# Optimization experiments

Measured on AMD Instinct MI355X. Metric: run time of the kernel, lower is better.

The kernel has to match this reference:

```python
import jax, jax.numpy as jnp
import numpy as np

N = 100000      # nodes
E = 3200000     # edges (avg degree 32)
NFEAT, NHID, NCLASS = 512, 256, 64


def setup_inputs() -> dict:
    key = jax.random.key(0)
    ks = jax.random.split(key, 10)
    x = jax.random.normal(ks[0], (N, NFEAT), dtype=jnp.float32)
    src = jax.random.randint(ks[1], (E,), 0, N, dtype=jnp.int32)
    dst = jax.random.randint(ks[2], (E,), 0, N, dtype=jnp.int32)
    # normalized-adjacency-style positive edge weights
    edge_weight = jax.random.uniform(ks[3], (E,), dtype=jnp.float32) / 32.0
    stdv1 = 1.0 / np.sqrt(NHID)
    stdv2 = 1.0 / np.sqrt(NCLASS)
    W1 = jax.random.uniform(ks[4], (NFEAT, NHID), minval=-stdv1, maxval=stdv1, dtype=jnp.float32)
    b1 = jnp.zeros((NHID,), jnp.float32)
    W2 = jax.random.uniform(ks[5], (NHID, NCLASS), minval=-stdv2, maxval=stdv2, dtype=jnp.float32)
    b2 = jnp.zeros((NCLASS,), jnp.float32)
    W3 = jax.random.uniform(ks[6], (NCLASS, NCLASS), minval=-stdv2, maxval=stdv2, dtype=jnp.float32)
    r = jax.random.normal(ks[7], (NCLASS,), dtype=jnp.float32) * 0.05
    return {"x": x, "src": src, "dst": dst, "edge_weight": edge_weight,
            "W1": W1, "b1": b1, "W2": W2, "b2": b2, "W3": W3, "r": r}


def _spmm(h, src, dst, w, n):
    # adj @ h where adj[dst, src] = w  (sparse COO)
    msgs = h[src] * w[:, None]            # [E, d] gather + scale
    return jax.ops.segment_sum(msgs, dst, num_segments=n)  # scatter-add


def reference(x, src, dst, edge_weight, W1, b1, W2, b2, W3, r):
    n = x.shape[0]
    # gc1: relu(adj @ (x @ W1) + b1); dropout is identity in eval mode
    h = jax.nn.relu(_spmm(x @ W1, src, dst, edge_weight, n) + b1)
    # gc2: adj @ (h @ W2) + b2
    h = _spmm(h @ W2, src, dst, edge_weight, n) + b2
    # TransE-style layer: adj @ (h @ W3) + r  (learned translation vector)
    h = _spmm(h @ W3, src, dst, edge_weight, n) + r
    return jax.nn.log_softmax(h, axis=1)
```

## Files before the change

### kernel.cpp

```cpp
#include <hip/hip_runtime.h>
#include <math.h>


typedef __bf16 bf16x8 __attribute__((ext_vector_type(8)));
typedef __bf16 bf16x4 __attribute__((ext_vector_type(4)));
typedef float f32x4 __attribute__((ext_vector_type(4)));
typedef float f32x2 __attribute__((ext_vector_type(2)));


#define TILE 2048

__global__ __launch_bounds__(1024) void bucket_scatter(const int* __restrict__ src,
                                                       const int* __restrict__ dst,
                                                       const float* __restrict__ ew,
                                                       int* __restrict__ gcnt,
                                                       int2* __restrict__ tb,
                                                       int E, int buckcap) {
    __shared__ int hist[256];
    __shared__ int hscan[256];
    __shared__ int gbase[256];
    __shared__ int2 stage[TILE];
    __shared__ unsigned char sbuck[TILE];
    int tid = threadIdx.x;
    int e0 = blockIdx.x * TILE;
    int tilecnt = min(TILE, E - e0);
    if (tid < 256) hist[tid] = 0;
    __syncthreads();
    int myb[2], myr[2], key[2], mw[2];
#pragma unroll
    for (int u = 0; u < 2; ++u) {
        int e = e0 + u * 1024 + tid;
        myb[u] = -1;
        if (e < E) {
            int d = dst[e];
            int b = d >> 9;
            key[u] = (src[e] << 9) | (d & 511);
            mw[u] = __float_as_int(ew[e]);
            myb[u] = b;
            myr[u] = atomicAdd(&hist[b], 1);
        }
    }
    __syncthreads();
    if (tid < 256) {
        hscan[tid] = hist[tid];
        gbase[tid] = (hist[tid] > 0) ? atomicAdd(&gcnt[tid], hist[tid]) : 0;
    }
    __syncthreads();
    for (int off = 1; off < 256; off <<= 1) {
        int t = 0;
        if (tid < 256 && tid >= off) t = hscan[tid - off];
        __syncthreads();
        if (tid < 256) hscan[tid] += t;
        __syncthreads();
    }
#pragma unroll
    for (int u = 0; u < 2; ++u) {
        if (myb[u] >= 0) {
            int b = myb[u];
            int p = hscan[b] - hist[b] + myr[u];
            stage[p] = make_int2(key[u], mw[u]);
            sbuck[p] = (unsigned char)b;
        }
    }
    __syncthreads();
    for (int i = tid; i < tilecnt; i += 1024) {
        int2 ent = stage[i];
        int b = sbuck[i];
        int exc = hscan[b] - hist[b];
        tb[(size_t)b * buckcap + gbase[b] + (i - exc)] = ent;
    }
}

__global__ __launch_bounds__(1024) void bucket_place(const int2* __restrict__ tb,
                                                     const int* __restrict__ gcnt,
                                                     int* __restrict__ rp,
                                                     int2* __restrict__ ep,
                                                     int N, int buckcap) {
    __shared__ int h[512];
    __shared__ int cursor[512];
    __shared__ int gs[256];
    int b = blockIdx.x;
    int base = b << 9;
    int nn = min(512, N - base);
    int tid = threadIdx.x;
    if (tid < 512) h[tid] = 0;
    if (tid < 256) gs[tid] = gcnt[tid];
    __syncthreads();
    for (int off = 1; off < 256; off <<= 1) {
        int t = (tid < 256 && tid >= off) ? gs[tid - off] : 0;
        __syncthreads();
        if (tid < 256) gs[tid] += t;
        __syncthreads();
    }
    int cb = gcnt[b];
    int bo = gs[b] - cb;
    if (b == 0 && tid == 0) rp[N] = gs[255];
    const int2* tbb = tb + (size_t)b * buckcap;
    for (int i = tid; i < cb; i += 1024)
        atomicAdd(&h[((unsigned)tbb[i].x) & 511], 1);
    __syncthreads();
    if (tid < 512) cursor[tid] = h[tid];
    __syncthreads();
    for (int off = 1; off < 512; off <<= 1) {
        int t = (tid < 512 && tid >= off) ? cursor[tid - off] : 0;
        __syncthreads();
        if (tid < 512) cursor[tid] += t;
        __syncthreads();
    }
    if (tid < 512) {
        int excl = cursor[tid] - h[tid] + bo;
        cursor[tid] = excl;
        if (tid < nn) rp[base + tid] = excl;
    }
    __syncthreads();
    for (int i = tid; i < cb; i += 1024) {
        int2 e = tbb[i];
        int pos = atomicAdd(&cursor[((unsigned)e.x) & 511], 1);
        ep[pos] = make_int2((int)(((unsigned)e.x) >> 9), e.y);
    }
}


__global__ __launch_bounds__(256) void cast_transpose(const float* __restrict__ W,
                                                      __bf16* __restrict__ WT,
                                                      int K, int Nn) {
    int i = blockIdx.x * 256 + threadIdx.x;
    if (i < K * Nn) {
        int k = i / Nn, n = i % Nn;
        WT[(size_t)n * K + k] = (__bf16)W[i];
    }
}

__global__ __launch_bounds__(256) void make_w23t(const float* __restrict__ W2,
                                                 const float* __restrict__ W3,
                                                 const float* __restrict__ b2,
                                                 __bf16* __restrict__ W23T,
                                                 float* __restrict__ cvec) {
    int idx = blockIdx.x * 256 + threadIdx.x;
    int n = idx & 63, k = idx >> 6;
    float s = 0.f;
    for (int j = 0; j < 64; ++j) s = fmaf(W2[k * 64 + j], W3[j * 64 + n], s);
    W23T[n * 256 + k] = (__bf16)s;
    if (idx < 64) {
        float t = 0.f;
        for (int j = 0; j < 64; ++j) t = fmaf(b2[j], W3[j * 64 + idx], t);
        cvec[idx] = t;
    }
}


__global__ __launch_bounds__(512) void gemm1_fused(const float* __restrict__ A,
                                                   const __bf16* __restrict__ BT,
                                                   unsigned char* __restrict__ C, int M) {
    const int K = 512;
    __shared__ __align__(16) __bf16 As[128 * 40];
    __shared__ __align__(16) __bf16 Bs[256 * 40];
    const int tid = threadIdx.x;
    const int wave = tid >> 6, lane = tid & 63;
    const int wm = wave >> 2, wn = wave & 3;
    const int quad = lane >> 4, l16 = lane & 15;
    const int bm = blockIdx.x * 128;
    f32x4 acc[4][4] = {};
    for (int k0 = 0; k0 < K; k0 += 32) {
#pragma unroll
        for (int it = 0; it < 2; ++it) {
            int idx = tid + it * 512;
            int row = idx >> 3, ch = idx & 7;
            int gm = bm + row;
            float4 v = (gm < M) ? *(const float4*)(A + (size_t)gm * K + k0 + ch * 4)
                                : make_float4(0.f, 0.f, 0.f, 0.f);
            bf16x4 o;
            o[0] = (__bf16)v.x; o[1] = (__bf16)v.y; o[2] = (__bf16)v.z; o[3] = (__bf16)v.w;
            *(bf16x4*)(As + row * 40 + ch * 4) = o;
        }
#pragma unroll
        for (int it = 0; it < 2; ++it) {
            int idx = tid + it * 512;
            int row = idx >> 2, ch = idx & 3;
            *(bf16x8*)(Bs + row * 40 + ch * 8) =
                *(const bf16x8*)(BT + (size_t)row * K + k0 + ch * 8);
        }
        __syncthreads();
        bf16x8 a[4], b[4];
#pragma unroll
        for (int i = 0; i < 4; ++i)
            a[i] = *(bf16x8*)(As + (wm * 64 + i * 16 + l16) * 40 + quad * 8);
#pragma unroll
        for (int j = 0; j < 4; ++j)
            b[j] = *(bf16x8*)(Bs + (wn * 64 + j * 16 + l16) * 40 + quad * 8);
#pragma unroll
        for (int i = 0; i < 4; ++i)
#pragma unroll
            for (int j = 0; j < 4; ++j)
                acc[i][j] = __builtin_amdgcn_mfma_f32_16x16x32_bf16(a[i], b[j], acc[i][j], 0, 0, 0);
        __syncthreads();
    }
#pragma unroll
    for (int i = 0; i < 4; ++i)
#pragma unroll
        for (int j = 0; j < 4; ++j)
#pragma unroll
            for (int rr = 0; rr < 4; ++rr) {
                int row = bm + wm * 64 + i * 16 + quad * 4 + rr;
                int col = wn * 64 + j * 16 + l16;
                if (row < M) {
                    unsigned int p = __builtin_amdgcn_cvt_pk_fp8_f32(acc[i][j][rr],
                                                                     acc[i][j][rr], 0, false);
                    C[(size_t)row * 256 + col] = (unsigned char)(p & 0xff);
                }
            }
}


__global__ __launch_bounds__(256) void gemm2_mfma(const __bf16* __restrict__ A,
                                                  const __bf16* __restrict__ BT,
                                                  __bf16* __restrict__ C, int M) {
    const int K = 256, Nn = 64;
    __shared__ __align__(16) __bf16 Bs[64 * 264];
    __shared__ __align__(16) __bf16 As[128 * 40];
    const int tid = threadIdx.x;
    const int wave = tid >> 6, lane = tid & 63;
    const int quad = lane >> 4, l16 = lane & 15;
    const int bm = blockIdx.x * 128;
#pragma unroll
    for (int it = 0; it < 8; ++it) {
        int e = tid + it * 256;
        int row = e >> 5, ch = e & 31;
        *(bf16x8*)(Bs + row * 264 + ch * 8) = *(const bf16x8*)(BT + row * 256 + ch * 8);
    }
    f32x4 acc[2][4] = {};
    for (int k0 = 0; k0 < K; k0 += 32) {
#pragma unroll
        for (int it = 0; it < 2; ++it) {
            int e = tid + it * 256;
            int row = e >> 2, ch = e & 3;
            int gm = bm + row;
            bf16x8 v = {};
            if (gm < M) v = *(const bf16x8*)(A + (size_t)gm * K + k0 + ch * 8);
            *(bf16x8*)(As + row * 40 + ch * 8) = v;
        }
        __syncthreads();
        bf16x8 a[2], b[4];
#pragma unroll
        for (int i = 0; i < 2; ++i)
            a[i] = *(bf16x8*)(As + (wave * 32 + i * 16 + l16) * 40 + quad * 8);
#pragma unroll
        for (int j = 0; j < 4; ++j)
            b[j] = *(bf16x8*)(Bs + (j * 16 + l16) * 264 + k0 + quad * 8);
#pragma unroll
        for (int i = 0; i < 2; ++i)
#pragma unroll
            for (int j = 0; j < 4; ++j)
                acc[i][j] = __builtin_amdgcn_mfma_f32_16x16x32_bf16(a[i], b[j], acc[i][j], 0, 0, 0);
        __syncthreads();
    }
#pragma unroll
    for (int i = 0; i < 2; ++i)
#pragma unroll
        for (int j = 0; j < 4; ++j)
#pragma unroll
            for (int rr = 0; rr < 4; ++rr) {
                int row = bm + wave * 32 + i * 16 + quad * 4 + rr;
                int col = j * 16 + l16;
                if (row < M) C[(size_t)row * Nn + col] = (__bf16)acc[i][j][rr];
            }
}


__global__ __launch_bounds__(256) void spmm256_fp8(const unsigned char* __restrict__ h,
                                                   const int* __restrict__ rp,
                                                   const int2* __restrict__ ep,
                                                   const float* __restrict__ bias,
                                                   __bf16* __restrict__ out, int n) {
    int node = blockIdx.x * 4 + (threadIdx.x >> 6);
    if (node >= n) return;
    int lane = threadIdx.x & 63;
    int q = lane >> 4, c = lane & 15;
    int e0 = rp[node], e1 = rp[node + 1];
    float acc[16] = {};
    for (int e = e0; e < e1; e += 16) {
#pragma unroll
        for (int u = 0; u < 4; ++u) {
            int ee = e + u * 4 + q;
            int cl = min(ee, e1 - 1);
            int2 p = ep[cl];
            float w = (ee < e1) ? __int_as_float(p.y) : 0.f;
            uint4 v = *(const uint4*)(h + (size_t)p.x * 256 + c * 16);
            f32x2 f;
            f = __builtin_amdgcn_cvt_pk_f32_fp8(v.x, false);
            acc[0] = fmaf(w, f.x, acc[0]);  acc[1] = fmaf(w, f.y, acc[1]);
            f = __builtin_amdgcn_cvt_pk_f32_fp8(v.x, true);
            acc[2] = fmaf(w, f.x, acc[2]);  acc[3] = fmaf(w, f.y, acc[3]);
            f = __builtin_amdgcn_cvt_pk_f32_fp8(v.y, false);
            acc[4] = fmaf(w, f.x, acc[4]);  acc[5] = fmaf(w, f.y, acc[5]);
            f = __builtin_amdgcn_cvt_pk_f32_fp8(v.y, true);
            acc[6] = fmaf(w, f.x, acc[6]);  acc[7] = fmaf(w, f.y, acc[7]);
            f = __builtin_amdgcn_cvt_pk_f32_fp8(v.z, false);
            acc[8] = fmaf(w, f.x, acc[8]);  acc[9] = fmaf(w, f.y, acc[9]);
            f = __builtin_amdgcn_cvt_pk_f32_fp8(v.z, true);
            acc[10] = fmaf(w, f.x, acc[10]); acc[11] = fmaf(w, f.y, acc[11]);
            f = __builtin_amdgcn_cvt_pk_f32_fp8(v.w, false);
            acc[12] = fmaf(w, f.x, acc[12]); acc[13] = fmaf(w, f.y, acc[13]);
            f = __builtin_amdgcn_cvt_pk_f32_fp8(v.w, true);
            acc[14] = fmaf(w, f.x, acc[14]); acc[15] = fmaf(w, f.y, acc[15]);
        }
    }
#pragma unroll
    for (int off = 16; off <= 32; off <<= 1)
#pragma unroll
        for (int i = 0; i < 16; ++i) acc[i] += __shfl_xor(acc[i], off);
    if (q == 0) {
        float4 b0 = *(const float4*)(bias + c * 16);
        float4 b1 = *(const float4*)(bias + c * 16 + 4);
        float4 b2 = *(const float4*)(bias + c * 16 + 8);
        float4 b3 = *(const float4*)(bias + c * 16 + 12);
        bf16x8 o0, o1;
        o0[0] = (__bf16)fmaxf(acc[0] + b0.x, 0.f);
        o0[1] = (__bf16)fmaxf(acc[1] + b0.y, 0.f);
        o0[2] = (__bf16)fmaxf(acc[2] + b0.z, 0.f);
        o0[3] = (__bf16)fmaxf(acc[3] + b0.w, 0.f);
        o0[4] = (__bf16)fmaxf(acc[4] + b1.x, 0.f);
        o0[5] = (__bf16)fmaxf(acc[5] + b1.y, 0.f);
        o0[6] = (__bf16)fmaxf(acc[6] + b1.z, 0.f);
        o0[7] = (__bf16)fmaxf(acc[7] + b1.w, 0.f);
        o1[0] = (__bf16)fmaxf(acc[8] + b2.x, 0.f);
        o1[1] = (__bf16)fmaxf(acc[9] + b2.y, 0.f);
        o1[2] = (__bf16)fmaxf(acc[10] + b2.z, 0.f);
        o1[3] = (__bf16)fmaxf(acc[11] + b2.w, 0.f);
        o1[4] = (__bf16)fmaxf(acc[12] + b3.x, 0.f);
        o1[5] = (__bf16)fmaxf(acc[13] + b3.y, 0.f);
        o1[6] = (__bf16)fmaxf(acc[14] + b3.z, 0.f);
        o1[7] = (__bf16)fmaxf(acc[15] + b3.w, 0.f);
        *(bf16x8*)(out + (size_t)node * 256 + c * 16) = o0;
        *(bf16x8*)(out + (size_t)node * 256 + c * 16 + 8) = o1;
    }
}

__global__ __launch_bounds__(1024) void spmm64_a(const __bf16* __restrict__ h,
                                                 const int* __restrict__ rp,
                                                 const int2* __restrict__ ep,
                                                 __bf16* __restrict__ out,
                                                 float* __restrict__ degw, int n) {
    __shared__ int2 eps[16][128];
    int wave = threadIdx.x >> 6;
    int node = blockIdx.x * 16 + wave;
    if (node >= n) return;
    int lane = threadIdx.x & 63;
    int g = lane >> 3, c = lane & 7;
    int e0 = rp[node], e1 = rp[node + 1];
    int deg = e1 - e0;
    for (int k = lane; k < min(deg, 128); k += 64) eps[wave][k] = ep[e0 + k];
    f32x2 acc2[4] = {};
    float ws = 0.f;
    auto run = [&](auto fetch) {
        for (int e = 0; e < deg; e += 32) {
#pragma unroll
            for (int u = 0; u < 4; ++u) {
                int s = e + u * 8 + g;
                int k = min(s, deg - 1);
                int2 p = fetch(k);
                float wv = (s < deg) ? __int_as_float(p.y) : 0.f;
                f32x2 w2 = {wv, wv};
                uint4 v = *(const uint4*)(h + (size_t)p.x * 64 + c * 8);
                f32x2 f;
                f = f32x2{__uint_as_float(v.x << 16), __uint_as_float(v.x & 0xffff0000u)};
                acc2[0] = __builtin_elementwise_fma(w2, f, acc2[0]);
                f = f32x2{__uint_as_float(v.y << 16), __uint_as_float(v.y & 0xffff0000u)};
                acc2[1] = __builtin_elementwise_fma(w2, f, acc2[1]);
                f = f32x2{__uint_as_float(v.z << 16), __uint_as_float(v.z & 0xffff0000u)};
                acc2[2] = __builtin_elementwise_fma(w2, f, acc2[2]);
                f = f32x2{__uint_as_float(v.w << 16), __uint_as_float(v.w & 0xffff0000u)};
                acc2[3] = __builtin_elementwise_fma(w2, f, acc2[3]);
                ws += wv;
            }
        }
    };
    if (deg <= 128) run([&](int k) { return eps[wave][k]; });
    else           run([&](int k) { return ep[e0 + k]; });
#pragma unroll
    for (int off = 8; off <= 32; off <<= 1) {
        ws += __shfl_xor(ws, off);
#pragma unroll
        for (int i = 0; i < 4; ++i) {
            acc2[i].x += __shfl_xor(acc2[i].x, off);
            acc2[i].y += __shfl_xor(acc2[i].y, off);
        }
    }
    if (lane == 0) degw[node] = ws;
    if (g == 0) {
        bf16x8 o;
#pragma unroll
        for (int i = 0; i < 4; ++i) {
            o[2 * i] = (__bf16)acc2[i].x;
            o[2 * i + 1] = (__bf16)acc2[i].y;
        }
        *(bf16x8*)(out + (size_t)node * 64 + c * 8) = o;
    }
}

__global__ __launch_bounds__(1024) void spmm64_b(const __bf16* __restrict__ h,
                                                 const int* __restrict__ rp,
                                                 const int2* __restrict__ ep,
                                                 const float* __restrict__ degw,
                                                 const float* __restrict__ cvec,
                                                 const float* __restrict__ r,
                                                 float* __restrict__ out, int n) {
    __shared__ int2 eps[16][128];
    int wave = threadIdx.x >> 6;
    int node = blockIdx.x * 16 + wave;
    if (node >= n) return;
    int lane = threadIdx.x & 63;
    int g = lane >> 3, c = lane & 7;
    int e0 = rp[node], e1 = rp[node + 1];
    int deg = e1 - e0;
    for (int k = lane; k < min(deg, 128); k += 64) eps[wave][k] = ep[e0 + k];
    f32x2 acc2[4] = {};
    auto run = [&](auto fetch) {
        for (int e = 0; e < deg; e += 32) {
#pragma unroll
            for (int u = 0; u < 4; ++u) {
                int s = e + u * 8 + g;
                int k = min(s, deg - 1);
                int2 p = fetch(k);
                float wv = (s < deg) ? __int_as_float(p.y) : 0.f;
                f32x2 w2 = {wv, wv};
                uint4 v = *(const uint4*)(h + (size_t)p.x * 64 + c * 8);
                f32x2 f;
                f = f32x2{__uint_as_float(v.x << 16), __uint_as_float(v.x & 0xffff0000u)};
                acc2[0] = __builtin_elementwise_fma(w2, f, acc2[0]);
                f = f32x2{__uint_as_float(v.y << 16), __uint_as_float(v.y & 0xffff0000u)};
                acc2[1] = __builtin_elementwise_fma(w2, f, acc2[1]);
                f = f32x2{__uint_as_float(v.z << 16), __uint_as_float(v.z & 0xffff0000u)};
                acc2[2] = __builtin_elementwise_fma(w2, f, acc2[2]);
                f = f32x2{__uint_as_float(v.w << 16), __uint_as_float(v.w & 0xffff0000u)};
                acc2[3] = __builtin_elementwise_fma(w2, f, acc2[3]);
            }
        }
    };
    if (deg <= 128) run([&](int k) { return eps[wave][k]; });
    else           run([&](int k) { return ep[e0 + k]; });
#pragma unroll
    for (int off = 8; off <= 32; off <<= 1)
#pragma unroll
        for (int i = 0; i < 4; ++i) {
            acc2[i].x += __shfl_xor(acc2[i].x, off);
            acc2[i].y += __shfl_xor(acc2[i].y, off);
        }
    float dw = degw[node];
    float4 c0 = *(const float4*)(cvec + c * 8), c1 = *(const float4*)(cvec + c * 8 + 4);
    float4 r0 = *(const float4*)(r + c * 8),    r1 = *(const float4*)(r + c * 8 + 4);
    float v[8];
    v[0] = acc2[0].x + dw * c0.x + r0.x; v[1] = acc2[0].y + dw * c0.y + r0.y;
    v[2] = acc2[1].x + dw * c0.z + r0.z; v[3] = acc2[1].y + dw * c0.w + r0.w;
    v[4] = acc2[2].x + dw * c1.x + r1.x; v[5] = acc2[2].y + dw * c1.y + r1.y;
    v[6] = acc2[3].x + dw * c1.z + r1.z; v[7] = acc2[3].y + dw * c1.w + r1.w;
    float m = v[0];
#pragma unroll
    for (int i = 1; i < 8; ++i) m = fmaxf(m, v[i]);
#pragma unroll
    for (int off = 1; off <= 4; off <<= 1) m = fmaxf(m, __shfl_xor(m, off));
    float s = 0.f;
#pragma unroll
    for (int i = 0; i < 8; ++i) s += __expf(v[i] - m);
#pragma unroll
    for (int off = 1; off <= 4; off <<= 1) s += __shfl_xor(s, off);
    float ls = m + __logf(s);
    if (g == 0) {
        float4 o0 = make_float4(v[0] - ls, v[1] - ls, v[2] - ls, v[3] - ls);
        float4 o1 = make_float4(v[4] - ls, v[5] - ls, v[6] - ls, v[7] - ls);
        *(float4*)(out + (size_t)node * 64 + c * 8) = o0;
        *(float4*)(out + (size_t)node * 64 + c * 8 + 4) = o1;
    }
}


extern "C" void kernel_launch(void* const* d_in, const int* in_sizes, int n_in,
                              void* d_out, int out_size, void* d_ws, size_t ws_size,
                              hipStream_t stream) {
    const float* x   = (const float*)d_in[0];
    const int*   src = (const int*)d_in[1];
    const int*   dst = (const int*)d_in[2];
    const float* ew  = (const float*)d_in[3];
    const float* W1  = (const float*)d_in[4];
    const float* b1  = (const float*)d_in[5];
    const float* W2  = (const float*)d_in[6];
    const float* b2  = (const float*)d_in[7];
    const float* W3  = (const float*)d_in[8];
    const float* r   = (const float*)d_in[9];

    const int N = in_sizes[0] / 512;
    const int E = in_sizes[1];
    const int NB = (N + 511) >> 9;
    const int buckcap = (((E / NB) * 5) / 4 + 255) & ~255;

    char* ws = (char*)d_ws;
    __bf16* h1 = (__bf16*)ws;
    char* regB = ws + (size_t)N * 512;
    unsigned char* h0f = (unsigned char*)regB;
    __bf16* g3   = (__bf16*)regB;
    __bf16* t1   = (__bf16*)(regB + (size_t)N * 128);
    float*  degw = (float*)(regB + (size_t)N * 256);
    char* regC = regB + (size_t)N * 512;
    __bf16* W1T  = (__bf16*)regC;
    __bf16* W23T = (__bf16*)(regC + 512 * 256 * 2);
    float*  cvec = (float*)(regC + 512 * 256 * 2 + 64 * 256 * 2);
    char* regD = regC + 512 * 1024;
    int*  rp   = (int*)regD;
    int*  gcnt = rp + (N + 2);
    int*  boff = gcnt + 256;
    int2* ep   = (int2*)(boff + 256);
    int2* tb   = ep + E;

    hipMemsetAsync(gcnt, 0, 256 * sizeof(int), stream);
    bucket_scatter<<<(E + TILE - 1) / TILE, 1024, 0, stream>>>(src, dst, ew,
                                                               gcnt, tb, E, buckcap);
    bucket_place<<<NB, 1024, 0, stream>>>(tb, gcnt, rp, ep, N, buckcap);

    cast_transpose<<<(512 * 256 + 255) / 256, 256, 0, stream>>>(W1, W1T, 512, 256);
    make_w23t<<<64, 256, 0, stream>>>(W2, W3, b2, W23T, cvec);

    gemm1_fused<<<(N + 127) / 128, 512, 0, stream>>>(x, W1T, h0f, N);
    spmm256_fp8<<<(N + 3) / 4, 256, 0, stream>>>(h0f, rp, ep, b1, h1, N);

    gemm2_mfma<<<(N + 127) / 128, 256, 0, stream>>>(h1, W23T, g3, N);
    spmm64_a<<<(N + 15) / 16, 1024, 0, stream>>>(g3, rp, ep, t1, degw, N);
    spmm64_b<<<(N + 15) / 16, 1024, 0, stream>>>(t1, rp, ep, degw, cvec, r, (float*)d_out, N);
}
```

Measured before the change: 687.0 us.

## Merge preprocessing kernels and run bucket placement alongside first GEMM

Folds the W1 cast-transpose and the W2·W3 product into the bucket-scatter launch as extra block ranges. Bucket placement and the first GEMM now share one launch, split by block index. This removes three kernel launches and lets the independent CSR build overlap with the dense GEMM. The cost is a shared-memory footprint set by the larger role, which may lower occupancy, and placement blocks now run with 512 threads instead of 1024.

```diff
diff --git a/kernel.cpp b/kernel.cpp
--- a/kernel.cpp
+++ b/kernel.cpp
@@ -7,22 +7,51 @@
 typedef float f32x4 __attribute__((ext_vector_type(4)));
 typedef float f32x2 __attribute__((ext_vector_type(2)));
 
-
 #define TILE 2048
-
-__global__ __launch_bounds__(1024) void bucket_scatter(const int* __restrict__ src,
-                                                       const int* __restrict__ dst,
-                                                       const float* __restrict__ ew,
-                                                       int* __restrict__ gcnt,
-                                                       int2* __restrict__ tb,
-                                                       int E, int buckcap) {
-    __shared__ int hist[256];
-    __shared__ int hscan[256];
-    __shared__ int gbase[256];
-    __shared__ int2 stage[TILE];
-    __shared__ unsigned char sbuck[TILE];
+#define PRE_BLKS 144
+
+
+__global__ __launch_bounds__(1024) void prep_scatter(const int* __restrict__ src,
+                                                     const int* __restrict__ dst,
+                                                     const float* __restrict__ ew,
+                                                     int* __restrict__ gcnt,
+                                                     int2* __restrict__ tb,
+                                                     int E, int buckcap,
+                                                     const float* __restrict__ W1,
+                                                     __bf16* __restrict__ W1T,
+                                                     const float* __restrict__ W2,
+                                                     const float* __restrict__ W3,
+                                                     const float* __restrict__ b2,
+                                                     __bf16* __restrict__ W23T,
+                                                     float* __restrict__ cvec) {
+    __shared__ __align__(16) char smem[21504];
+    int bx = blockIdx.x;
     int tid = threadIdx.x;
-    int e0 = blockIdx.x * TILE;
+    if (bx < 128) {
+        int i = bx * 1024 + tid;
+        int k = i >> 8, n = i & 255;
+        W1T[n * 512 + k] = (__bf16)W1[i];
+        return;
+    }
+    if (bx < PRE_BLKS) {
+        int idx = (bx - 128) * 1024 + tid;
+        int n = idx & 63, k = idx >> 6;
+        float s = 0.f;
+        for (int j = 0; j < 64; ++j) s = fmaf(W2[k * 64 + j], W3[j * 64 + n], s);
+        W23T[n * 256 + k] = (__bf16)s;
+        if (idx < 64) {
+            float t = 0.f;
+            for (int j = 0; j < 64; ++j) t = fmaf(b2[j], W3[j * 64 + idx], t);
+            cvec[idx] = t;
+        }
+        return;
+    }
+    int* hist  = (int*)smem;
+    int* hscan = hist + 256;
+    int* gbase = hscan + 256;
+    int2* stage = (int2*)(gbase + 256);
+    unsigned char* sbuck = (unsigned char*)(stage + TILE);
+    int e0 = (bx - PRE_BLKS) * TILE;
     int tilecnt = min(TILE, E - e0);
     if (tid < 256) hist[tid] = 0;
     __syncthreads();
@@ -71,95 +100,68 @@
     }
 }
 
-__global__ __launch_bounds__(1024) void bucket_place(const int2* __restrict__ tb,
-                                                     const int* __restrict__ gcnt,
-                                                     int* __restrict__ rp,
-                                                     int2* __restrict__ ep,
-                                                     int N, int buckcap) {
-    __shared__ int h[512];
-    __shared__ int cursor[512];
-    __shared__ int gs[256];
-    int b = blockIdx.x;
-    int base = b << 9;
-    int nn = min(512, N - base);
-    int tid = threadIdx.x;
-    if (tid < 512) h[tid] = 0;
-    if (tid < 256) gs[tid] = gcnt[tid];
-    __syncthreads();
-    for (int off = 1; off < 256; off <<= 1) {
-        int t = (tid < 256 && tid >= off) ? gs[tid - off] : 0;
-        __syncthreads();
-        if (tid < 256) gs[tid] += t;
-        __syncthreads();
-    }
-    int cb = gcnt[b];
-    int bo = gs[b] - cb;
-    if (b == 0 && tid == 0) rp[N] = gs[255];
-    const int2* tbb = tb + (size_t)b * buckcap;
-    for (int i = tid; i < cb; i += 1024)
-        atomicAdd(&h[((unsigned)tbb[i].x) & 511], 1);
-    __syncthreads();
-    if (tid < 512) cursor[tid] = h[tid];
-    __syncthreads();
-    for (int off = 1; off < 512; off <<= 1) {
-        int t = (tid < 512 && tid >= off) ? cursor[tid - off] : 0;
-        __syncthreads();
-        if (tid < 512) cursor[tid] += t;
-        __syncthreads();
-    }
-    if (tid < 512) {
+
+__global__ __launch_bounds__(512) void place_gemm1(const int2* __restrict__ tb,
+                                                   const int* __restrict__ gcnt,
+                                                   int* __restrict__ rp,
+                                                   int2* __restrict__ ep,
+                                                   int N, int buckcap,
+                                                   const float* __restrict__ A,
+                                                   const __bf16* __restrict__ BT,
+                                                   unsigned char* __restrict__ C) {
+    __shared__ __align__(16) char smem[30720];
+    const int tid = threadIdx.x;
+    const int bx = blockIdx.x;
+    const int NBp = (N + 511) >> 9;
+    if (bx < NBp) {
+        int* h = (int*)smem;
+        int* cursor = h + 512;
+        int* gs = cursor + 512;
+        int b = bx;
+        int base = b << 9;
+        int nn = min(512, N - base);
+        h[tid] = 0;
+        if (tid < 256) gs[tid] = gcnt[tid];
+        __syncthreads();
+        for (int off = 1; off < 256; off <<= 1) {
+            int t = (tid < 256 && tid >= off) ? gs[tid - off] : 0;
+            __syncthreads();
+            if (tid < 256) gs[tid] += t;
+            __syncthreads();
+        }
+        int cb = gcnt[b];
+        int bo = gs[b] - cb;
+        if (b == 0 && tid == 0) rp[N] = gs[255];
+        const int2* tbb = tb + (size_t)b * buckcap;
+        for (int i = tid; i < cb; i += 512)
+            atomicAdd(&h[((unsigned)tbb[i].x) & 511], 1);
+        __syncthreads();
+        cursor[tid] = h[tid];
+        __syncthreads();
+        for (int off = 1; off < 512; off <<= 1) {
+            int t = (tid >= off) ? cursor[tid - off] : 0;
+            __syncthreads();
+            cursor[tid] += t;
+            __syncthreads();
+        }
         int excl = cursor[tid] - h[tid] + bo;
         cursor[tid] = excl;
         if (tid < nn) rp[base + tid] = excl;
-    }
-    __syncthreads();
-    for (int i = tid; i < cb; i += 1024) {
-        int2 e = tbb[i];
-        int pos = atomicAdd(&cursor[((unsigned)e.x) & 511], 1);
-        ep[pos] = make_int2((int)(((unsigned)e.x) >> 9), e.y);
-    }
-}
-
-
-__global__ __launch_bounds__(256) void cast_transpose(const float* __restrict__ W,
-                                                      __bf16* __restrict__ WT,
-                                                      int K, int Nn) {
-    int i = blockIdx.x * 256 + threadIdx.x;
-    if (i < K * Nn) {
-        int k = i / Nn, n = i % Nn;
-        WT[(size_t)n * K + k] = (__bf16)W[i];
-    }
-}
-
-__global__ __launch_bounds__(256) void make_w23t(const float* __restrict__ W2,
-                                                 const float* __restrict__ W3,
-                                                 const float* __restrict__ b2,
-                                                 __bf16* __restrict__ W23T,
-                                                 float* __restrict__ cvec) {
-    int idx = blockIdx.x * 256 + threadIdx.x;
-    int n = idx & 63, k = idx >> 6;
-    float s = 0.f;
-    for (int j = 0; j < 64; ++j) s = fmaf(W2[k * 64 + j], W3[j * 64 + n], s);
-    W23T[n * 256 + k] = (__bf16)s;
-    if (idx < 64) {
-        float t = 0.f;
-        for (int j = 0; j < 64; ++j) t = fmaf(b2[j], W3[j * 64 + idx], t);
-        cvec[idx] = t;
-    }
-}
-
-
-__global__ __launch_bounds__(512) void gemm1_fused(const float* __restrict__ A,
-                                                   const __bf16* __restrict__ BT,
-                                                   unsigned char* __restrict__ C, int M) {
-    const int K = 512;
-    __shared__ __align__(16) __bf16 As[128 * 40];
-    __shared__ __align__(16) __bf16 Bs[256 * 40];
-    const int tid = threadIdx.x;
+        __syncthreads();
+        for (int i = tid; i < cb; i += 512) {
+            int2 e = tbb[i];
+            int pos = atomicAdd(&cursor[((unsigned)e.x) & 511], 1);
+            ep[pos] = make_int2((int)(((unsigned)e.x) >> 9), e.y);
+        }
+        return;
+    }
+    const int K = 512, M = N;
+    __bf16* As = (__bf16*)smem;
+    __bf16* Bs = As + 128 * 40;
     const int wave = tid >> 6, lane = tid & 63;
     const int wm = wave >> 2, wn = wave & 3;
     const int quad = lane >> 4, l16 = lane & 15;
-    const int bm = blockIdx.x * 128;
+    const int bm = (bx - NBp) * 128;
     f32x4 acc[4][4] = {};
     for (int k0 = 0; k0 < K; k0 += 32) {
 #pragma unroll
@@ -512,14 +514,12 @@
     int2* tb   = ep + E;
 
     hipMemsetAsync(gcnt, 0, 256 * sizeof(int), stream);
-    bucket_scatter<<<(E + TILE - 1) / TILE, 1024, 0, stream>>>(src, dst, ew,
-                                                               gcnt, tb, E, buckcap);
-    bucket_place<<<NB, 1024, 0, stream>>>(tb, gcnt, rp, ep, N, buckcap);
-
-    cast_transpose<<<(512 * 256 + 255) / 256, 256, 0, stream>>>(W1, W1T, 512, 256);
-    make_w23t<<<64, 256, 0, stream>>>(W2, W3, b2, W23T, cvec);
-
-    gemm1_fused<<<(N + 127) / 128, 512, 0, stream>>>(x, W1T, h0f, N);
+    prep_scatter<<<PRE_BLKS + (E + TILE - 1) / TILE, 1024, 0, stream>>>(
+        src, dst, ew, gcnt, tb, E, buckcap, W1, W1T, W2, W3, b2, W23T, cvec);
+
+    place_gemm1<<<NB + (N + 127) / 128, 512, 0, stream>>>(
+        tb, gcnt, rp, ep, N, buckcap, x, W1T, h0f);
+
     spmm256_fp8<<<(N + 3) / 4, 256, 0, stream>>>(h0f, rp, ep, b1, h1, N);
 
     gemm2_mfma<<<(N + 127) / 128, 256, 0, stream>>>(h1, W23T, g3, N);
```

New measurement: 654.8 us. -4.7%, faster.
